# Kernel tuning notes

Hardware: AMD Instinct MI355X
Metric: run time of the kernel (lower is better)

The kernel has to match this reference:

```python
import jax, jax.numpy as jnp
import numpy as np

NUM_EXPERTS = 16
TOP_K = 2
FFT_LEN = 512
SEQ_LEN = 512
PRED_LEN = 720
MOE_TEMP = 1.0


def setup_inputs() -> dict:
    key = jax.random.key(0)
    ks = jax.random.split(key, 5)
    x = jax.random.normal(ks[0], (8192, SEQ_LEN), dtype=jnp.float32)
    # gating network: Linear(fft_len//2 -> num_experts)
    gw = jax.random.normal(ks[1], (NUM_EXPERTS, FFT_LEN // 2), dtype=jnp.float32) * (1.0 / np.sqrt(FFT_LEN // 2))
    gb = jnp.zeros((NUM_EXPERTS,), dtype=jnp.float32)
    # experts: RLinear = instance-norm (RevIN) + Linear(seq->pred), stacked
    ew = jax.random.normal(ks[2], (NUM_EXPERTS, SEQ_LEN, PRED_LEN), dtype=jnp.float32) * (1.0 / np.sqrt(SEQ_LEN))
    eb = jnp.zeros((NUM_EXPERTS, PRED_LEN), dtype=jnp.float32)
    return {"x": x, "gw": gw, "gb": gb, "ew": ew, "eb": eb}


def periodogram(x, n):
    # x: [B, L] -> normalized power spectrum [B, n//2]
    x0 = x - jnp.mean(x, axis=1, keepdims=True)
    dft = jnp.fft.fft(x0, n=n, axis=1) / jnp.sqrt(jnp.asarray(n, x.dtype))
    I = jnp.abs(dft[:, : n // 2]) ** 2
    s = jnp.sum(I, axis=1, keepdims=True)
    s = jnp.where(s == 0, 1.0, s)
    return I / s


def expert_apply(x, ew, eb):
    # RLinear: instance normalize, linear map, de-normalize
    mu = jnp.mean(x, axis=1, keepdims=True)
    sd = jnp.std(x, axis=1, keepdims=True) + 1e-5
    xn = (x - mu) / sd  # [B, L]
    # all experts densely: [B,L] x [E,L,P] -> [E,B,P]
    y = jnp.einsum('bl,elp->ebp', xn, ew) + eb[:, None, :]
    return y * sd[None] + mu[None]  # [E, B, P]


def reference(x, gw, gb, ew, eb):
    I = periodogram(x, FFT_LEN)  # [B, n//2]
    gate = (I @ gw.T + gb) / MOE_TEMP  # eval mode: divide by temp, no noise
    topk_vals, topk_idx = jax.lax.top_k(gate, TOP_K)  # [B, k]
    gates = jax.nn.softmax(topk_vals, axis=1)  # [B, k]
    expert_out = expert_apply(x, ew, eb)  # [E, B, P]
    # gather selected experts: [B, k, P]
    sel = jnp.take_along_axis(
        jnp.transpose(expert_out, (1, 0, 2)), topk_idx[:, :, None], axis=1
    )
    return jnp.sum(gates[:, :, None] * sel, axis=1)  # [B, P]
```

## Files before the change

### kernel.cpp

```cpp
#include <hip/hip_runtime.h>
#include <hip/hip_bf16.h>
#include <math.h>

#define NEXP  16
#define SEQ   512
#define PRED  720
#define NROWS 8192
#define NFREQ 256

typedef __bf16 bf16x8 __attribute__((ext_vector_type(8)));
typedef float  f32x16 __attribute__((ext_vector_type(16)));

__device__ __forceinline__ void gload_lds16(const void* g, void* l) {
    __builtin_amdgcn_global_load_lds(
        (const __attribute__((address_space(1))) unsigned int*)g,
        (__attribute__((address_space(3))) unsigned int*)l, 16, 0, 0);
}

__device__ __forceinline__ int xcd_swizzle(int bid, int nwg) {
    const int q = nwg >> 3, r = nwg & 7;
    const int xcd = bid & 7, off = bid >> 3;
    return (xcd < r ? xcd * (q + 1) : r * (q + 1) + (xcd - r) * q) + off;
}

__global__ __launch_bounds__(256) void k_transpose_ew(const float* __restrict__ ew,
                                                      __hip_bfloat16* __restrict__ ewt)
{
    __shared__ float tile[32][33];
    const int e  = blockIdx.z;
    const int p0 = blockIdx.x * 32;
    const int l0 = blockIdx.y * 32;
    const int tx = threadIdx.x & 31;
    const int ty = threadIdx.x >> 5;
    const float* src = ew + (size_t)e * SEQ * PRED;
#pragma unroll
    for (int i = 0; i < 4; ++i) {
        int l = l0 + ty + i * 8;
        int p = p0 + tx;
        tile[ty + i * 8][tx] = (p < PRED) ? src[(size_t)l * PRED + p] : 0.f;
    }
    __syncthreads();
    __hip_bfloat16* dst = ewt + (size_t)e * PRED * SEQ;
#pragma unroll
    for (int i = 0; i < 4; ++i) {
        int p = p0 + ty + i * 8;
        int l = l0 + tx;
        if (p < PRED) dst[(size_t)p * SEQ + l] = __float2bfloat16(tile[tx][ty + i * 8]);
    }
}

__global__ __launch_bounds__(256) void k_build_dft(__hip_bfloat16* __restrict__ bthi,
                                                   __hip_bfloat16* __restrict__ btlo,
                                                   int* __restrict__ nredo)
{
    if (blockIdx.x == 0 && threadIdx.x == 0) *nredo = 0;

    const int tid  = blockIdx.x * 256 + threadIdx.x;
    const int f    = tid >> 9;
    const int lidx = tid & 511;
    const int m    = (f * lidx) & 511;

    constexpr double Cj[9] = {0.9999247018391445033, 0.9996988186962042201,
                              0.9987954562051723927, 0.9951847266721968862,
                              0.9807852804032304491, 0.9238795325112867561,
                              0.7071067811865475244, 0.0, -1.0};
    constexpr double Sj[9] = {0.0122715382857199261, 0.0245412285229122880,
                              0.0490676743274180143, 0.0980171403295606020,
                              0.1950903220161282678, 0.3826834323650897717,
                              0.7071067811865475244, 1.0, 0.0};
    double cr = 1.0, ci = 0.0;
#pragma unroll
    for (int j = 0; j < 9; ++j) {
        const bool on = (m >> j) & 1;
        const double mr = on ? Cj[j] : 1.0;
        const double mi = on ? Sj[j] : 0.0;
        const double nr = cr * mr - ci * mi;
        ci = cr * mi + ci * mr;
        cr = nr;
    }

    const size_t c0 = (size_t)(2 * f) * 512 + lidx;
    const size_t c1 = (size_t)(2 * f + 1) * 512 + lidx;
    {
        __hip_bfloat16 h = __float2bfloat16((float)cr);
        float hif = __bfloat162float(h);
        bthi[c0] = h;
        btlo[c0] = __float2bfloat16((float)(cr - (double)hif));
    }
    {
        __hip_bfloat16 h = __float2bfloat16((float)ci);
        float hif = __bfloat162float(h);
        bthi[c1] = h;
        btlo[c1] = __float2bfloat16((float)(ci - (double)hif));
    }
}

__global__ __launch_bounds__(256) void k_stats(const float* __restrict__ x,
                                               __hip_bfloat16* __restrict__ xn,
                                               __hip_bfloat16* __restrict__ xnlo,
                                               float* __restrict__ meta)
{
    const int t  = threadIdx.x;
    const int wv = t >> 6, l = t & 63;
    const int b  = blockIdx.x * 4 + wv;
    const float* xr = x + (size_t)b * SEQ;

    const float4 v0 = *(const float4*)(xr + l * 8);
    const float4 v1 = *(const float4*)(xr + l * 8 + 4);
    const double d0 = v0.x, d1 = v0.y, d2 = v0.z, d3 = v0.w;
    const double d4 = v1.x, d5 = v1.y, d6 = v1.z, d7 = v1.w;

    double s1 = ((d0 + d1) + (d2 + d3)) + ((d4 + d5) + (d6 + d7));
    double s2 = ((d0 * d0 + d1 * d1) + (d2 * d2 + d3 * d3)) +
                ((d4 * d4 + d5 * d5) + (d6 * d6 + d7 * d7));
#pragma unroll
    for (int off = 1; off < 64; off <<= 1) {
        s1 += __shfl_xor(s1, off);
        s2 += __shfl_xor(s2, off);
    }
    const double mu = s1 * (1.0 / 512.0);
    double var = s2 * (1.0 / 512.0) - mu * mu;
    if (var < 0.0) var = 0.0;
    const double sd = sqrt(var) + 1e-5, inv = 1.0 / sd;

    unsigned int hw[4], lw[4];
#define CONV(j, dj)                                                         \
    {                                                                       \
        double xnd = (dj - mu) * inv;                                       \
        __hip_bfloat16 h = __float2bfloat16((float)xnd);                    \
        float hif = __bfloat162float(h);                                    \
        __hip_bfloat16 lo = __float2bfloat16((float)(xnd - (double)hif));   \
        unsigned int hb = *(unsigned short*)&h;                             \
        unsigned int lb = *(unsigned short*)&lo;                            \
        if ((j & 1) == 0) { hw[j >> 1] = hb; lw[j >> 1] = lb; }             \
        else { hw[j >> 1] |= hb << 16; lw[j >> 1] |= lb << 16; }            \
    }
    CONV(0, d0) CONV(1, d1) CONV(2, d2) CONV(3, d3)
    CONV(4, d4) CONV(5, d5) CONV(6, d6) CONV(7, d7)
#undef CONV
    *(uint4*)(xn   + (size_t)b * SEQ + l * 8) = uint4{hw[0], hw[1], hw[2], hw[3]};
    *(uint4*)(xnlo + (size_t)b * SEQ + l * 8) = uint4{lw[0], lw[1], lw[2], lw[3]};

    if (l == 0) {
        meta[b * 4 + 0] = (float)mu;
        meta[b * 4 + 3] = (float)sd;
    }
}

__global__ __launch_bounds__(256, 3) void k_dft_gemm(
    const __hip_bfloat16* __restrict__ xn, const __hip_bfloat16* __restrict__ xnlo,
    const __hip_bfloat16* __restrict__ bthi, const __hip_bfloat16* __restrict__ btlo,
    float* __restrict__ Iout)
{
    const int wgid = xcd_swizzle(blockIdx.x, 512);
    const int rt = wgid >> 2;
    const int ct = wgid & 3;

    __shared__ __align__(16) __hip_bfloat16 As[2][64][64];
    __shared__ __align__(16) __hip_bfloat16 Bs[2][128][64];

    const int t  = threadIdx.x;
    const int wv = t >> 6, l = t & 63;
    const int trow = t >> 3, tchk = t & 7;

    size_t aoff[2], boff[4];
#pragma unroll
    for (int i = 0; i < 2; ++i) {
        const int r   = i * 32 + trow;
        const int swz = (r & 7) ^ ((r & 8) >> 1);
        aoff[i] = (size_t)(rt * 64 + r) * SEQ + (size_t)(tchk ^ swz) * 8;
    }
#pragma unroll
    for (int i = 0; i < 4; ++i) {
        const int r   = i * 32 + trow;
        const int swz = (r & 7) ^ ((r & 8) >> 1);
        boff[i] = (size_t)(ct * 128 + r) * SEQ + (size_t)(tchk ^ swz) * 8;
    }

#define DSTAGE(buf, kk) do {                                                   \
    const int pass_ = (kk) >> 3;                                               \
    const int koff_ = ((kk) & 7) * 64;                                         \
    const __hip_bfloat16* ap_ = (pass_ == 1) ? xnlo : xn;                      \
    const __hip_bfloat16* bp_ = (pass_ == 2) ? btlo : bthi;                    \
    _Pragma("unroll")                                                          \
    for (int i_ = 0; i_ < 2; ++i_)                                             \
        gload_lds16(ap_ + aoff[i_] + koff_, &As[buf][i_ * 32 + wv * 8][0]);    \
    _Pragma("unroll")                                                          \
    for (int i_ = 0; i_ < 4; ++i_)                                             \
        gload_lds16(bp_ + boff[i_] + koff_, &Bs[buf][i_ * 32 + wv * 8][0]);    \
} while (0)

    f32x16 acc[2];
#pragma unroll
    for (int ni = 0; ni < 2; ++ni)
#pragma unroll
        for (int q = 0; q < 16; ++q) acc[ni][q] = 0.f;

    const int wr = wv >> 1, wc = wv & 1;
    const int fl = l & 31, fh = l >> 5;
    const int rswz = (fl & 7) ^ ((fl & 8) >> 1);

    DSTAGE(0, 0);
    DSTAGE(1, 1);
    for (int kt = 0; kt < 24; ++kt) {
        const int cur = kt & 1;
        if (kt < 23) asm volatile("s_waitcnt vmcnt(6)" ::: "memory");
        else         asm volatile("s_waitcnt vmcnt(0)" ::: "memory");
        __builtin_amdgcn_sched_barrier(0);
        __builtin_amdgcn_s_barrier();
        __builtin_amdgcn_sched_barrier(0);
#pragma unroll
        for (int ks = 0; ks < 4; ++ks) {
            const int g  = ks * 2 + fh;
            const int cc = (g ^ rswz) * 8;
            const bf16x8 a  = *(const bf16x8*)&As[cur][wr * 32 + fl][cc];
            const bf16x8 b0 = *(const bf16x8*)&Bs[cur][wc * 64 + fl][cc];
            const bf16x8 b1 = *(const bf16x8*)&Bs[cur][wc * 64 + 32 + fl][cc];
            acc[0] = __builtin_amdgcn_mfma_f32_32x32x16_bf16(a, b0, acc[0], 0, 0, 0);
            acc[1] = __builtin_amdgcn_mfma_f32_32x32x16_bf16(a, b1, acc[1], 0, 0, 0);
        }
        __builtin_amdgcn_sched_barrier(0);
        __builtin_amdgcn_s_barrier();
        __builtin_amdgcn_sched_barrier(0);
        if (kt + 2 < 24) DSTAGE(cur, kt + 2);
    }
#undef DSTAGE

    const int crow_base = 4 * fh;
#pragma unroll
    for (int ni = 0; ni < 2; ++ni) {
        const int col = ct * 128 + wc * 64 + ni * 32 + fl;
#pragma unroll
        for (int q = 0; q < 16; ++q) {
            const float v = acc[ni][q];
            const float w = __shfl_xor(v, 1);
            if ((fl & 1) == 0) {
                const int rl = wr * 32 + (q & 3) + 8 * (q >> 2) + crow_base;
                Iout[(size_t)(rt * 64 + rl) * NFREQ + (col >> 1)] = v * v + w * w;
            }
        }
    }
}

__global__ __launch_bounds__(256) void k_gatefin(const float* __restrict__ Iout,
                                                 const float* __restrict__ gw,
                                                 const float* __restrict__ gb,
                                                 float* __restrict__ meta,
                                                 int* __restrict__ eidx,
                                                 int* __restrict__ redo,
                                                 int* __restrict__ nredo)
{
    __shared__ float gws[NEXP * 257];
    __shared__ float Pw[4][256];
    __shared__ float Gs[4][16];

    const int t  = threadIdx.x;
    const int wv = t >> 6, l = t & 63;
    const int b  = blockIdx.x * 4 + wv;

    for (int i = t; i < NEXP * NFREQ; i += 256)
        gws[(i >> 8) * 257 + (i & 255)] = gw[i];
    __syncthreads();

    const float* Ir = Iout + (size_t)b * NFREQ;
    const float i0 = Ir[l], i1 = Ir[64 + l], i2 = Ir[128 + l], i3 = Ir[192 + l];
    Pw[wv][l] = i0; Pw[wv][64 + l] = i1; Pw[wv][128 + l] = i2; Pw[wv][192 + l] = i3;
    float ps = (i0 + i1) + (i2 + i3);
#pragma unroll
    for (int off = 1; off < 64; off <<= 1) ps += __shfl_xor(ps, off);

    const int e = l >> 2, kb = l & 3;
    float acc = 0.f;
#pragma unroll 8
    for (int j = 0; j < 64; ++j) {
        const int k = kb + 4 * j;
        acc += Pw[wv][k] * gws[e * 257 + k];
    }
    acc += __shfl_xor(acc, 1);
    acc += __shfl_xor(acc, 2);
    if (kb == 0) Gs[wv][e] = acc;

    if (l == 0) {
        const float sdiv  = (ps == 0.f) ? 1.f : ps;
        const float inv_s = 1.f / sdiv;
        float b1 = -1e30f, b2 = -1e30f, b3 = -1e30f;
        int i1b = 0, i2b = 0;
#pragma unroll
        for (int i = 0; i < NEXP; ++i) {
            float v = Gs[wv][i] * inv_s + gb[i];
            if (v > b1)      { b3 = b2; b2 = b1; i2b = i1b; b1 = v; i1b = i; }
            else if (v > b2) { b3 = b2; b2 = v; i2b = i; }
            else if (v > b3) { b3 = v; }
        }
        if (b2 - b3 < 1e-4f * fmaxf(1.f, fabsf(b1))) {
            const int r = atomicAdd(nredo, 1);
            redo[r] = b;
        } else {
            const float sd = meta[b * 4 + 3];
            const float ee = __expf(b2 - b1);
            const float w0 = 1.f / (1.f + ee);
            const float w1 = ee / (1.f + ee);
            meta[b * 4 + 1] = w0 * sd;
            meta[b * 4 + 2] = w1 * sd;
            eidx[b * 2 + 0] = i1b;
            eidx[b * 2 + 1] = i2b;
        }
    }
}

__global__ __launch_bounds__(256, 4) void k_gate64(const float* __restrict__ x,
                                                   const float* __restrict__ gw,
                                                   const float* __restrict__ gb,
                                                   float* __restrict__ meta,
                                                   int* __restrict__ eidx,
                                                   const int* __restrict__ redo,
                                                   const int* __restrict__ nredo)
{
    __shared__ double Pw[4][256];
    __shared__ double Gs[4][16];

    const int t  = threadIdx.x;
    const int wv = t >> 6, l = t & 63;
    const int n  = *nredo;

    for (int it = blockIdx.x * 4 + wv; it < n; it += gridDim.x * 4) {
        const int b = redo[it];
        const float* xr = x + (size_t)b * SEQ;

        double s1 = 0.0, s2 = 0.0;
#define DLOADV(n_) double vr##n_ = (double)xr[64 * n_ + l]; s1 += vr##n_; s2 += vr##n_ * vr##n_;
        DLOADV(0) DLOADV(1) DLOADV(2) DLOADV(3) DLOADV(4) DLOADV(5) DLOADV(6) DLOADV(7)
#undef DLOADV
        double vi0, vi1, vi2, vi3, vi4, vi5, vi6, vi7;

#pragma unroll
        for (int off = 1; off < 64; off <<= 1) {
            s1 += __shfl_xor(s1, off);
            s2 += __shfl_xor(s2, off);
        }
        const double mu = s1 * (1.0 / 512.0);
        double var = s2 * (1.0 / 512.0) - mu * mu;
        if (var < 0.0) var = 0.0;
        const double sd = sqrt(var) + 1e-5;

#define DSUB(n_) vr##n_ -= mu;
        DSUB(0) DSUB(1) DSUB(2) DSUB(3) DSUB(4) DSUB(5) DSUB(6) DSUB(7)
#undef DSUB

        {
            const double C = 0.70710678118654752440084436210485;
            double a0 = vr0 + vr4, a1 = vr1 + vr5, a2 = vr2 + vr6, a3 = vr3 + vr7;
            double d0 = vr0 - vr4, d1 = vr1 - vr5, d2 = vr2 - vr6, d3 = vr3 - vr7;
            double c0 = a0 + a2, c2 = a0 - a2, c1 = a1 + a3;
            double c3i = a3 - a1;
            double e1r = C * (d1 - d3), e1i = -C * (d1 + d3);
            vr0 = c0 + c1;   vi0 = 0.0;
            vr1 = c0 - c1;   vi1 = 0.0;
            vr2 = c2;        vi2 = c3i;
            vr3 = c2;        vi3 = -c3i;
            vr4 = d0 + e1r;  vi4 = -d2 + e1i;
            vr5 = d0 - e1r;  vi5 = -d2 - e1i;
            vr6 = d0 - e1r;  vi6 =  d2 + e1i;
            vr7 = d0 + e1r;  vi7 =  d2 - e1i;
        }

        double w1r = 1.0, w1i = 0.0;
        {
            constexpr double Cr[6] = {0.9999247018391445033, 0.9996988186962042201,
                                      0.9987954562051723927, 0.9951847266721968862,
                                      0.9807852804032304491, 0.9238795325112867561};
            constexpr double Ci[6] = {-0.0122715382857199261, -0.0245412285229122880,
                                      -0.0490676743274180143, -0.0980171403295606020,
                                      -0.1950903220161282678, -0.3826834323650897717};
#pragma unroll
            for (int j = 0; j < 6; ++j) {
                const bool on = (l >> j) & 1;
                const double mr = on ? Cr[j] : 1.0;
                const double mi = on ? Ci[j] : 0.0;
                const double nr = w1r * mr - w1i * mi;
                w1i = w1r * mi + w1i * mr;
                w1r = nr;
            }
        }

        {
            double wkr = w1r, wki = w1i;
#define DTWID(n_) { double tr_ = vr##n_ * wkr - vi##n_ * wki; \
                    vi##n_ = vr##n_ * wki + vi##n_ * wkr; vr##n_ = tr_; }
#define DWSTEP() { double nr_ = wkr * w1r - wki * w1i; \
                   wki = wkr * w1i + wki * w1r; wkr = nr_; }
            DTWID(4) DWSTEP() DTWID(2) DWSTEP() DTWID(6) DWSTEP() DTWID(1)
            DWSTEP() DTWID(5) DWSTEP() DTWID(3) DWSTEP() DTWID(7)
#undef DTWID
#undef DWSTEP
        }

        double twr, twi;
        {
            double w2r = w1r * w1r - w1i * w1i, w2i = 2.0 * w1r * w1i;
            double w4r = w2r * w2r - w2i * w2i, w4i = 2.0 * w2r * w2i;
            twr = w4r * w4r - w4i * w4i; twi = 2.0 * w4r * w4i;
        }
#define DBF(R, I, h, hi, ter, tei) { \
        double br_ = __shfl_xor(R, h); double bi_ = __shfl_xor(I, h); \
        double dr_ = hi ? (R - br_) : (R + br_); \
        double di_ = hi ? (I - bi_) : (I + bi_); \
        R = dr_ * ter - di_ * tei; I = dr_ * tei + di_ * ter; }
#define DSTAGE(hc) { \
        const bool hi_ = (l & hc) != 0; \
        const double ter_ = hi_ ? twr : 1.0; \
        const double tei_ = hi_ ? twi : 0.0; \
        DBF(vr0, vi0, hc, hi_, ter_, tei_) DBF(vr1, vi1, hc, hi_, ter_, tei_) \
        DBF(vr2, vi2, hc, hi_, ter_, tei_) DBF(vr3, vi3, hc, hi_, ter_, tei_) \
        DBF(vr4, vi4, hc, hi_, ter_, tei_) DBF(vr5, vi5, hc, hi_, ter_, tei_) \
        DBF(vr6, vi6, hc, hi_, ter_, tei_) DBF(vr7, vi7, hc, hi_, ter_, tei_) \
        double ntr_ = twr * twr - twi * twi; twi = 2.0 * twr * twi; twr = ntr_; }
        DSTAGE(32) DSTAGE(16) DSTAGE(8) DSTAGE(4) DSTAGE(2) DSTAGE(1)
#undef DSTAGE
#undef DBF

        const int k2 = (int)(__brev((unsigned)l) >> 26);
        double ps = 0.0;
        if ((l & 1) == 0) {
            const int kb = 8 * k2;
            double P;
            P = vr0 * vr0 + vi0 * vi0; ps += P; Pw[wv][0 + kb] = P;
            P = vr1 * vr1 + vi1 * vi1; ps += P; Pw[wv][4 + kb] = P;
            P = vr2 * vr2 + vi2 * vi2; ps += P; Pw[wv][2 + kb] = P;
            P = vr3 * vr3 + vi3 * vi3; ps += P; Pw[wv][6 + kb] = P;
            P = vr4 * vr4 + vi4 * vi4; ps += P; Pw[wv][1 + kb] = P;
            P = vr5 * vr5 + vi5 * vi5; ps += P; Pw[wv][5 + kb] = P;
            P = vr6 * vr6 + vi6 * vi6; ps += P; Pw[wv][3 + kb] = P;
            P = vr7 * vr7 + vi7 * vi7; ps += P; Pw[wv][7 + kb] = P;
        }
#pragma unroll
        for (int off = 1; off < 64; off <<= 1) ps += __shfl_xor(ps, off);

        {
            const int e = l >> 2, kb = l & 3;
            double acc = 0.0;
#pragma unroll 8
            for (int j = 0; j < 64; ++j) {
                int k = kb + 4 * j;
                acc += Pw[wv][k] * (double)gw[e * NFREQ + k];
            }
            acc += __shfl_xor(acc, 1);
            acc += __shfl_xor(acc, 2);
            if (kb == 0) Gs[wv][e] = acc;
        }

        if (l == 0) {
            const double sdiv  = (ps == 0.0) ? 1.0 : ps;
            const double inv_s = 1.0 / sdiv;
            double best = -1e300, best2 = -1e300;
            int i0b = 0, i1b = 0;
#pragma unroll
            for (int i = 0; i < NEXP; ++i) {
                double v = Gs[wv][i] * inv_s + (double)gb[i];
                if (v > best)       { best2 = best; i1b = i0b; best = v; i0b = i; }
                else if (v > best2) { best2 = v; i1b = i; }
            }
            const double eexp = (double)__expf((float)(best2 - best));
            const double w0 = 1.0 / (1.0 + eexp);
            const double w1 = eexp / (1.0 + eexp);
            meta[b * 4 + 0] = (float)mu;
            meta[b * 4 + 1] = (float)(w0 * sd);
            meta[b * 4 + 2] = (float)(w1 * sd);
            meta[b * 4 + 3] = (float)sd;
            eidx[b * 2 + 0] = i0b;
            eidx[b * 2 + 1] = i1b;
        }
    }
}

__global__ __launch_bounds__(256) void k_count(const int* __restrict__ eidx,
                                               int* __restrict__ blockHist)
{
    __shared__ int h[32];
    const int t   = threadIdx.x;
    const int blk = blockIdx.x;
    if (t < 32) h[t] = 0;
    __syncthreads();
    const int b  = blk * 256 + t;
    const int e0 = eidx[2 * b];
    const int e1 = eidx[2 * b + 1];
    atomicAdd(&h[e0], 1);
    atomicAdd(&h[16 + e1], 1);
    __syncthreads();
    if (t < 32) blockHist[(t >> 4) * 512 + blk * 16 + (t & 15)] = h[t];
}

__global__ void k_scan(const int* __restrict__ blockHist, int* __restrict__ counts,
                       int* __restrict__ offs, int* __restrict__ toff,
                       int* __restrict__ base)
{
    __shared__ int cnt[32];
    __shared__ int off_s[32];
    const int j = threadIdx.x;
    if (j < 32) {
        const int s = j >> 4, e = j & 15;
        int acc = 0;
        for (int blk = 0; blk < 32; ++blk) acc += blockHist[s * 512 + blk * 16 + e];
        cnt[j] = acc;
        counts[j] = acc;
    }
    __syncthreads();
    if (j < 2) {
        int acc = 0, tac = 0;
        for (int i = 0; i < NEXP; ++i) {
            const int c = cnt[j * 16 + i];
            off_s[j * 16 + i] = acc;
            offs[j * 16 + i]  = acc;
            acc += c;
            toff[j * 17 + i] = tac;
            tac += (c + 63) >> 6;
        }
        toff[j * 17 + 16] = tac;
    }
    __syncthreads();
    if (j < 32) {
        const int s = j >> 4, e = j & 15;
        int run = off_s[j];
        for (int blk = 0; blk < 32; ++blk) {
            base[s * 512 + blk * 16 + e] = run;
            run += blockHist[s * 512 + blk * 16 + e];
        }
    }
}

__global__ __launch_bounds__(256) void k_scatter(const int* __restrict__ eidx,
                                                 const int* __restrict__ base,
                                                 int* __restrict__ lists)
{
    __shared__ int whist[2][4][16];
    const int t   = threadIdx.x;
    const int wv  = t >> 6, l = t & 63;
    const int blk = blockIdx.x;
    const int b   = blk * 256 + t;
    const int e0  = eidx[2 * b];
    const int e1  = eidx[2 * b + 1];
    const unsigned long long before = (1ULL << l) - 1ULL;

    unsigned long long m0 = 0, m1 = 0;
#pragma unroll
    for (int bb = 0; bb < 16; ++bb) {
        unsigned long long m = __ballot(e0 == bb);
        if (e0 == bb) m0 = m;
        if (l == 0) whist[0][wv][bb] = __popcll(m);
    }
#pragma unroll
    for (int bb = 0; bb < 16; ++bb) {
        unsigned long long m = __ballot(e1 == bb);
        if (e1 == bb) m1 = m;
        if (l == 0) whist[1][wv][bb] = __popcll(m);
    }
    __syncthreads();

    int p0 = __popcll(m0 & before);
    int p1 = __popcll(m1 & before);
    for (int w = 0; w < 4; ++w) {
        if (w < wv) {
            p0 += whist[0][w][e0];
            p1 += whist[1][w][e1];
        }
    }
    lists[base[blk * 16 + e0] + p0]                 = b;
    lists[NROWS + base[512 + blk * 16 + e1] + p1]   = b;
}

template <int SLOT>
__global__ __launch_bounds__(256, 3) void k_expert_gemm(
    const __hip_bfloat16* __restrict__ xn, const __hip_bfloat16* __restrict__ ewt,
    const float* __restrict__ eb, const float* __restrict__ meta,
    const int* __restrict__ lists, const int* __restrict__ offs,
    const int* __restrict__ counts, const int* __restrict__ toff,
    float* __restrict__ out)
{
    const int wgid = xcd_swizzle(blockIdx.x, 864);
    const int tid  = wgid / 6;
    const int ct   = wgid % 6;
    if (tid >= toff[SLOT * 17 + 16]) return;
    int e = 0;
#pragma unroll
    for (int i = 0; i < 15; ++i) e += (toff[SLOT * 17 + e + 1] <= tid) ? 1 : 0;
    const int rt  = tid - toff[SLOT * 17 + e];
    const int n_e = counts[SLOT * NEXP + e];

    __shared__ __align__(16) __hip_bfloat16 As[2][64][64];
    __shared__ __align__(16) __hip_bfloat16 Bs[2][128][64];
    __shared__ int   rowB[64];
    __shared__ float rowMu[64];
    __shared__ float rowC[64];

    const int t  = threadIdx.x;
    const int wv = t >> 6, l = t & 63;
    const int* list = lists + SLOT * NROWS + offs[SLOT * NEXP + e];
    if (t < 64) {
        int r  = rt * 64 + t;
        int bb = (r < n_e) ? list[r] : -1;
        rowB[t]  = bb;
        rowMu[t] = (bb >= 0) ? meta[bb * 4] : 0.f;
        rowC[t]  = (bb >= 0) ? meta[bb * 4 + 1 + SLOT] : 0.f;
    }
    __syncthreads();

    const int trow = t >> 3, tchk = t & 7;
    const __hip_bfloat16* asrc[2];
    const __hip_bfloat16* bsrc[4];
#pragma unroll
    for (int i = 0; i < 2; ++i) {
        const int r   = i * 32 + trow;
        const int swz = (r & 7) ^ ((r & 8) >> 1);
        const int ab  = rowB[r];
        asrc[i] = xn + ((ab >= 0) ? (size_t)ab * SEQ : 0) + (size_t)(tchk ^ swz) * 8;
    }
#pragma unroll
    for (int i = 0; i < 4; ++i) {
        const int r   = i * 32 + trow;
        const int swz = (r & 7) ^ ((r & 8) >> 1);
        const int gc  = ct * 128 + r;
        const int gcc = (gc < PRED) ? gc : (PRED - 1);
        bsrc[i] = ewt + ((size_t)e * PRED + gcc) * SEQ + (size_t)(tchk ^ swz) * 8;
    }

#define STAGE(buf, koff) do {                                              \
    _Pragma("unroll")                                                      \
    for (int i_ = 0; i_ < 2; ++i_)                                         \
        gload_lds16(asrc[i_] + (koff), &As[buf][i_ * 32 + wv * 8][0]);     \
    _Pragma("unroll")                                                      \
    for (int i_ = 0; i_ < 4; ++i_)                                         \
        gload_lds16(bsrc[i_] + (koff), &Bs[buf][i_ * 32 + wv * 8][0]);     \
} while (0)

    f32x16 acc[2];
#pragma unroll
    for (int ni = 0; ni < 2; ++ni)
#pragma unroll
        for (int q = 0; q < 16; ++q) acc[ni][q] = 0.f;

    const int wr = wv >> 1, wc = wv & 1;
    const int fl = l & 31, fh = l >> 5;
    const int rswz = (fl & 7) ^ ((fl & 8) >> 1);

    STAGE(0, 0);
    STAGE(1, 64);
    for (int kt = 0; kt < 8; ++kt) {
        const int cur = kt & 1;
        if (kt < 7) asm volatile("s_waitcnt vmcnt(6)" ::: "memory");
        else        asm volatile("s_waitcnt vmcnt(0)" ::: "memory");
        __builtin_amdgcn_sched_barrier(0);
        __builtin_amdgcn_s_barrier();
        __builtin_amdgcn_sched_barrier(0);
#pragma unroll
        for (int ks = 0; ks < 4; ++ks) {
            const int g  = ks * 2 + fh;
            const int cc = (g ^ rswz) * 8;
            const bf16x8 a  = *(const bf16x8*)&As[cur][wr * 32 + fl][cc];
            const bf16x8 b0 = *(const bf16x8*)&Bs[cur][wc * 64 + fl][cc];
            const bf16x8 b1 = *(const bf16x8*)&Bs[cur][wc * 64 + 32 + fl][cc];
            acc[0] = __builtin_amdgcn_mfma_f32_32x32x16_bf16(a, b0, acc[0], 0, 0, 0);
            acc[1] = __builtin_amdgcn_mfma_f32_32x32x16_bf16(a, b1, acc[1], 0, 0, 0);
        }
        __builtin_amdgcn_sched_barrier(0);
        __builtin_amdgcn_s_barrier();
        __builtin_amdgcn_sched_barrier(0);
        if (kt + 2 < 8) STAGE(cur, (kt + 2) * 64);
    }
#undef STAGE

    const int crow_base = 4 * fh;
#pragma unroll
    for (int ni = 0; ni < 2; ++ni) {
        const int col = ct * 128 + wc * 64 + ni * 32 + fl;
        const bool cok = (col < PRED);
        const float ebv = cok ? eb[e * PRED + col] : 0.f;
#pragma unroll
        for (int q = 0; q < 16; ++q) {
            const int rl = wr * 32 + (q & 3) + 8 * (q >> 2) + crow_base;
            const int bb = rowB[rl];
            if (!cok || bb < 0) continue;
            const float v = acc[ni][q] + ebv;
            float* op = out + (size_t)bb * PRED + col;
            if (SLOT == 0) *op = rowMu[rl] + rowC[rl] * v;
            else           *op += rowC[rl] * v;
        }
    }
}

extern "C" void kernel_launch(void* const* d_in, const int* in_sizes, int n_in,
                              void* d_out, int out_size, void* d_ws, size_t ws_size,
                              hipStream_t stream)
{
    const float* x  = (const float*)d_in[0];
    const float* gw = (const float*)d_in[1];
    const float* gb = (const float*)d_in[2];
    const float* ew = (const float*)d_in[3];
    const float* eb = (const float*)d_in[4];
    float* out = (float*)d_out;
    char*  ws  = (char*)d_ws;

    constexpr size_t XN_OFF   = 0;
    constexpr size_t XN_SZ    = (size_t)NROWS * SEQ * 2;
    constexpr size_t XNLO_OFF = XN_OFF + XN_SZ;
    constexpr size_t EWT_OFF  = XNLO_OFF + XN_SZ;
    constexpr size_t EWT_SZ   = (size_t)NEXP * PRED * SEQ * 2;
    constexpr size_t BTHI_OFF = EWT_OFF + EWT_SZ;
    constexpr size_t BT_SZ    = (size_t)512 * 512 * 2;
    constexpr size_t BTLO_OFF = BTHI_OFF + BT_SZ;
    constexpr size_t IOUT_OFF = BTLO_OFF + BT_SZ;
    constexpr size_t IOUT_SZ  = (size_t)NROWS * NFREQ * 4;
    constexpr size_t META_OFF = IOUT_OFF + IOUT_SZ;
    constexpr size_t META_SZ  = (size_t)NROWS * 4 * 4;
    constexpr size_t EIDX_OFF = META_OFF + META_SZ;
    constexpr size_t EIDX_SZ  = (size_t)NROWS * 2 * 4;
    constexpr size_t LIST_OFF = EIDX_OFF + EIDX_SZ;
    constexpr size_t LIST_SZ  = (size_t)2 * NROWS * 4;
    constexpr size_t CNT_OFF  = LIST_OFF + LIST_SZ;
    constexpr size_t OFFS_OFF = CNT_OFF + 144;
    constexpr size_t TOFF_OFF = OFFS_OFF + 128;
    constexpr size_t BH_OFF   = TOFF_OFF + 160;
    constexpr size_t BASE_OFF = BH_OFF + 4096;
    constexpr size_t REDO_OFF = BASE_OFF + 4096;

    __hip_bfloat16* xn   = (__hip_bfloat16*)(ws + XN_OFF);
    __hip_bfloat16* xnlo = (__hip_bfloat16*)(ws + XNLO_OFF);
    __hip_bfloat16* ewt  = (__hip_bfloat16*)(ws + EWT_OFF);
    __hip_bfloat16* bthi = (__hip_bfloat16*)(ws + BTHI_OFF);
    __hip_bfloat16* btlo = (__hip_bfloat16*)(ws + BTLO_OFF);
    float* Iout  = (float*)(ws + IOUT_OFF);
    float* meta  = (float*)(ws + META_OFF);
    int* eidx    = (int*)(ws + EIDX_OFF);
    int* lists   = (int*)(ws + LIST_OFF);
    int* counts  = (int*)(ws + CNT_OFF);
    int* nredo   = (int*)(ws + CNT_OFF + 128);
    int* offs    = (int*)(ws + OFFS_OFF);
    int* toff    = (int*)(ws + TOFF_OFF);
    int* bhist   = (int*)(ws + BH_OFF);
    int* base    = (int*)(ws + BASE_OFF);
    int* redo    = (int*)(ws + REDO_OFF);

    k_build_dft<<<dim3(512), dim3(256), 0, stream>>>(bthi, btlo, nredo);
    k_transpose_ew<<<dim3(23, 16, NEXP), dim3(256), 0, stream>>>(ew, ewt);
    k_stats<<<dim3(NROWS / 4), dim3(256), 0, stream>>>(x, xn, xnlo, meta);
    k_dft_gemm<<<dim3(512), dim3(256), 0, stream>>>(xn, xnlo, bthi, btlo, Iout);
    k_gatefin<<<dim3(NROWS / 4), dim3(256), 0, stream>>>(Iout, gw, gb, meta, eidx,
                                                         redo, nredo);
    k_gate64<<<dim3(64), dim3(256), 0, stream>>>(x, gw, gb, meta, eidx, redo, nredo);
    k_count<<<dim3(32), dim3(256), 0, stream>>>(eidx, bhist);
    k_scan<<<dim3(1), dim3(64), 0, stream>>>(bhist, counts, offs, toff, base);
    k_scatter<<<dim3(32), dim3(256), 0, stream>>>(eidx, base, lists);
    k_expert_gemm<0><<<dim3(864), dim3(256), 0, stream>>>(
        xn, ewt, eb, meta, lists, offs, counts, toff, out);
    k_expert_gemm<1><<<dim3(864), dim3(256), 0, stream>>>(
        xn, ewt, eb, meta, lists, offs, counts, toff, out);
}
```

Baseline: 154.0 us.

## Shrink GEMM tiles to 64x64 and use triple-buffered LDS with one barrier

Both the DFT GEMM and the expert GEMM go from 64x128 output tiles to 64x64, which doubles the grid size, and move from double to triple LDS buffering. With three buffers the second barrier after each compute step is dropped, so each k-step has one barrier and the prefetch can be two stages ahead. The cost is lower data reuse per block (each A tile is loaded twice as often) and one accumulator per wave instead of two, which means fewer MFMAs per LDS load.

```diff
diff --git a/kernel.cpp b/kernel.cpp
--- a/kernel.cpp
+++ b/kernel.cpp
@@ -152,29 +152,26 @@
     const __hip_bfloat16* __restrict__ bthi, const __hip_bfloat16* __restrict__ btlo,
     float* __restrict__ Iout)
 {
-    const int wgid = xcd_swizzle(blockIdx.x, 512);
-    const int rt = wgid >> 2;
-    const int ct = wgid & 3;
-
-    __shared__ __align__(16) __hip_bfloat16 As[2][64][64];
-    __shared__ __align__(16) __hip_bfloat16 Bs[2][128][64];
+    const int wgid = xcd_swizzle(blockIdx.x, 1024);
+    const int rt = wgid >> 3;
+    const int ct = wgid & 7;
+
+    __shared__ __align__(16) __hip_bfloat16 As[3][64][64];
+    __shared__ __align__(16) __hip_bfloat16 Bs[3][64][64];
 
     const int t  = threadIdx.x;
     const int wv = t >> 6, l = t & 63;
-    const int trow = t >> 3, tchk = t & 7;
-
-    size_t aoff[2], boff[4];
+
+    size_t aoff[2], boff[2];
+    int ldsrow[2], ldschk[2];
 #pragma unroll
     for (int i = 0; i < 2; ++i) {
-        const int r   = i * 32 + trow;
-        const int swz = (r & 7) ^ ((r & 8) >> 1);
-        aoff[i] = (size_t)(rt * 64 + r) * SEQ + (size_t)(tchk ^ swz) * 8;
-    }
-#pragma unroll
-    for (int i = 0; i < 4; ++i) {
-        const int r   = i * 32 + trow;
-        const int swz = (r & 7) ^ ((r & 8) >> 1);
-        boff[i] = (size_t)(ct * 128 + r) * SEQ + (size_t)(tchk ^ swz) * 8;
+        const int idx = i * 256 + t;
+        const int row = idx >> 3, chk = idx & 7;
+        const int swz = (row & 7) ^ ((row & 8) >> 1);
+        ldsrow[i] = row; ldschk[i] = chk;
+        aoff[i] = (size_t)(rt * 64 + row) * SEQ + (size_t)(chk ^ swz) * 8;
+        boff[i] = (size_t)(ct * 64 + row) * SEQ + (size_t)(chk ^ swz) * 8;
     }
 
 #define DSTAGE(buf, kk) do {                                                   \
@@ -184,17 +181,15 @@
     const __hip_bfloat16* bp_ = (pass_ == 2) ? btlo : bthi;                    \
     _Pragma("unroll")                                                          \
     for (int i_ = 0; i_ < 2; ++i_)                                             \
-        gload_lds16(ap_ + aoff[i_] + koff_, &As[buf][i_ * 32 + wv * 8][0]);    \
+        gload_lds16(ap_ + aoff[i_] + koff_, &As[buf][ldsrow[i_]][ldschk[i_] * 8]); \
     _Pragma("unroll")                                                          \
-    for (int i_ = 0; i_ < 4; ++i_)                                             \
-        gload_lds16(bp_ + boff[i_] + koff_, &Bs[buf][i_ * 32 + wv * 8][0]);    \
+    for (int i_ = 0; i_ < 2; ++i_)                                             \
+        gload_lds16(bp_ + boff[i_] + koff_, &Bs[buf][ldsrow[i_]][ldschk[i_] * 8]); \
 } while (0)
 
-    f32x16 acc[2];
-#pragma unroll
-    for (int ni = 0; ni < 2; ++ni)
-#pragma unroll
-        for (int q = 0; q < 16; ++q) acc[ni][q] = 0.f;
+    f32x16 acc;
+#pragma unroll
+    for (int q = 0; q < 16; ++q) acc[q] = 0.f;
 
     const int wr = wv >> 1, wc = wv & 1;
     const int fl = l & 31, fh = l >> 5;
@@ -202,42 +197,34 @@
 
     DSTAGE(0, 0);
     DSTAGE(1, 1);
+#pragma unroll
     for (int kt = 0; kt < 24; ++kt) {
-        const int cur = kt & 1;
-        if (kt < 23) asm volatile("s_waitcnt vmcnt(6)" ::: "memory");
+        const int cur = kt % 3;
+        if (kt < 23) asm volatile("s_waitcnt vmcnt(4)" ::: "memory");
         else         asm volatile("s_waitcnt vmcnt(0)" ::: "memory");
         __builtin_amdgcn_sched_barrier(0);
         __builtin_amdgcn_s_barrier();
         __builtin_amdgcn_sched_barrier(0);
 #pragma unroll
         for (int ks = 0; ks < 4; ++ks) {
-            const int g  = ks * 2 + fh;
-            const int cc = (g ^ rswz) * 8;
-            const bf16x8 a  = *(const bf16x8*)&As[cur][wr * 32 + fl][cc];
-            const bf16x8 b0 = *(const bf16x8*)&Bs[cur][wc * 64 + fl][cc];
-            const bf16x8 b1 = *(const bf16x8*)&Bs[cur][wc * 64 + 32 + fl][cc];
-            acc[0] = __builtin_amdgcn_mfma_f32_32x32x16_bf16(a, b0, acc[0], 0, 0, 0);
-            acc[1] = __builtin_amdgcn_mfma_f32_32x32x16_bf16(a, b1, acc[1], 0, 0, 0);
-        }
-        __builtin_amdgcn_sched_barrier(0);
-        __builtin_amdgcn_s_barrier();
-        __builtin_amdgcn_sched_barrier(0);
-        if (kt + 2 < 24) DSTAGE(cur, kt + 2);
+            const int cc = ((ks * 2 + fh) ^ rswz) * 8;
+            const bf16x8 a = *(const bf16x8*)&As[cur][wr * 32 + fl][cc];
+            const bf16x8 b = *(const bf16x8*)&Bs[cur][wc * 32 + fl][cc];
+            acc = __builtin_amdgcn_mfma_f32_32x32x16_bf16(a, b, acc, 0, 0, 0);
+        }
+        if (kt + 2 < 24) DSTAGE((kt + 2) % 3, kt + 2);
     }
 #undef DSTAGE
 
     const int crow_base = 4 * fh;
-#pragma unroll
-    for (int ni = 0; ni < 2; ++ni) {
-        const int col = ct * 128 + wc * 64 + ni * 32 + fl;
-#pragma unroll
-        for (int q = 0; q < 16; ++q) {
-            const float v = acc[ni][q];
-            const float w = __shfl_xor(v, 1);
-            if ((fl & 1) == 0) {
-                const int rl = wr * 32 + (q & 3) + 8 * (q >> 2) + crow_base;
-                Iout[(size_t)(rt * 64 + rl) * NFREQ + (col >> 1)] = v * v + w * w;
-            }
+    const int col = ct * 64 + wc * 32 + fl;
+#pragma unroll
+    for (int q = 0; q < 16; ++q) {
+        const float v = acc[q];
+        const float w = __shfl_xor(v, 1);
+        if ((fl & 1) == 0) {
+            const int rl = wr * 32 + (q & 3) + 8 * (q >> 2) + crow_base;
+            Iout[(size_t)(rt * 64 + rl) * NFREQ + (col >> 1)] = v * v + w * w;
         }
     }
 }
@@ -406,7 +393,7 @@
         double dr_ = hi ? (R - br_) : (R + br_); \
         double di_ = hi ? (I - bi_) : (I + bi_); \
         R = dr_ * ter - di_ * tei; I = dr_ * tei + di_ * ter; }
-#define DSTAGE(hc) { \
+#define DSTG(hc) { \
         const bool hi_ = (l & hc) != 0; \
         const double ter_ = hi_ ? twr : 1.0; \
         const double tei_ = hi_ ? twi : 0.0; \
@@ -415,8 +402,8 @@
         DBF(vr4, vi4, hc, hi_, ter_, tei_) DBF(vr5, vi5, hc, hi_, ter_, tei_) \
         DBF(vr6, vi6, hc, hi_, ter_, tei_) DBF(vr7, vi7, hc, hi_, ter_, tei_) \
         double ntr_ = twr * twr - twi * twi; twi = 2.0 * twr * twi; twr = ntr_; }
-        DSTAGE(32) DSTAGE(16) DSTAGE(8) DSTAGE(4) DSTAGE(2) DSTAGE(1)
-#undef DSTAGE
+        DSTG(32) DSTG(16) DSTG(8) DSTG(4) DSTG(2) DSTG(1)
+#undef DSTG
 #undef DBF
 
         const int k2 = (int)(__brev((unsigned)l) >> 26);
@@ -576,9 +563,9 @@
     const int* __restrict__ counts, const int* __restrict__ toff,
     float* __restrict__ out)
 {
-    const int wgid = xcd_swizzle(blockIdx.x, 864);
-    const int tid  = wgid / 6;
-    const int ct   = wgid % 6;
+    const int wgid = xcd_swizzle(blockIdx.x, 1728);
+    const int tid  = wgid / 12;
+    const int ct   = wgid % 12;
     if (tid >= toff[SLOT * 17 + 16]) return;
     int e = 0;
 #pragma unroll
@@ -586,8 +573,8 @@
     const int rt  = tid - toff[SLOT * 17 + e];
     const int n_e = counts[SLOT * NEXP + e];
 
-    __shared__ __align__(16) __hip_bfloat16 As[2][64][64];
-    __shared__ __align__(16) __hip_bfloat16 Bs[2][128][64];
+    __shared__ __align__(16) __hip_bfloat16 As[3][64][64];
+    __shared__ __align__(16) __hip_bfloat16 Bs[3][64][64];
     __shared__ int   rowB[64];
     __shared__ float rowMu[64];
     __shared__ float rowC[64];
@@ -604,39 +591,34 @@
     }
     __syncthreads();
 
-    const int trow = t >> 3, tchk = t & 7;
     const __hip_bfloat16* asrc[2];
-    const __hip_bfloat16* bsrc[4];
+    const __hip_bfloat16* bsrc[2];
+    int ldsrow[2], ldschk[2];
 #pragma unroll
     for (int i = 0; i < 2; ++i) {
-        const int r   = i * 32 + trow;
-        const int swz = (r & 7) ^ ((r & 8) >> 1);
-        const int ab  = rowB[r];
-        asrc[i] = xn + ((ab >= 0) ? (size_t)ab * SEQ : 0) + (size_t)(tchk ^ swz) * 8;
-    }
-#pragma unroll
-    for (int i = 0; i < 4; ++i) {
-        const int r   = i * 32 + trow;
-        const int swz = (r & 7) ^ ((r & 8) >> 1);
-        const int gc  = ct * 128 + r;
+        const int idx = i * 256 + t;
+        const int row = idx >> 3, chk = idx & 7;
+        const int swz = (row & 7) ^ ((row & 8) >> 1);
+        ldsrow[i] = row; ldschk[i] = chk;
+        const int ab  = rowB[row];
+        asrc[i] = xn + ((ab >= 0) ? (size_t)ab * SEQ : 0) + (size_t)(chk ^ swz) * 8;
+        const int gc  = ct * 64 + row;
         const int gcc = (gc < PRED) ? gc : (PRED - 1);
-        bsrc[i] = ewt + ((size_t)e * PRED + gcc) * SEQ + (size_t)(tchk ^ swz) * 8;
-    }
-
-#define STAGE(buf, koff) do {                                              \
-    _Pragma("unroll")                                                      \
-    for (int i_ = 0; i_ < 2; ++i_)                                         \
-        gload_lds16(asrc[i_] + (koff), &As[buf][i_ * 32 + wv * 8][0]);     \
-    _Pragma("unroll")                                                      \
-    for (int i_ = 0; i_ < 4; ++i_)                                         \
-        gload_lds16(bsrc[i_] + (koff), &Bs[buf][i_ * 32 + wv * 8][0]);     \
+        bsrc[i] = ewt + ((size_t)e * PRED + gcc) * SEQ + (size_t)(chk ^ swz) * 8;
+    }
+
+#define STAGE(buf, koff) do {                                                      \
+    _Pragma("unroll")                                                              \
+    for (int i_ = 0; i_ < 2; ++i_)                                                 \
+        gload_lds16(asrc[i_] + (koff), &As[buf][ldsrow[i_]][ldschk[i_] * 8]);      \
+    _Pragma("unroll")                                                              \
+    for (int i_ = 0; i_ < 2; ++i_)                                                 \
+        gload_lds16(bsrc[i_] + (koff), &Bs[buf][ldsrow[i_]][ldschk[i_] * 8]);      \
 } while (0)
 
-    f32x16 acc[2];
-#pragma unroll
-    for (int ni = 0; ni < 2; ++ni)
-#pragma unroll
-        for (int q = 0; q < 16; ++q) acc[ni][q] = 0.f;
+    f32x16 acc;
+#pragma unroll
+    for (int q = 0; q < 16; ++q) acc[q] = 0.f;
 
     const int wr = wv >> 1, wc = wv & 1;
     const int fl = l & 31, fh = l >> 5;
@@ -644,46 +626,38 @@
 
     STAGE(0, 0);
     STAGE(1, 64);
+#pragma unroll
     for (int kt = 0; kt < 8; ++kt) {
-        const int cur = kt & 1;
-        if (kt < 7) asm volatile("s_waitcnt vmcnt(6)" ::: "memory");
+        const int cur = kt % 3;
+        if (kt < 7) asm volatile("s_waitcnt vmcnt(4)" ::: "memory");
         else        asm volatile("s_waitcnt vmcnt(0)" ::: "memory");
         __builtin_amdgcn_sched_barrier(0);
         __builtin_amdgcn_s_barrier();
         __builtin_amdgcn_sched_barrier(0);
 #pragma unroll
         for (int ks = 0; ks < 4; ++ks) {
-            const int g  = ks * 2 + fh;
-            const int cc = (g ^ rswz) * 8;
-            const bf16x8 a  = *(const bf16x8*)&As[cur][wr * 32 + fl][cc];
-            const bf16x8 b0 = *(const bf16x8*)&Bs[cur][wc * 64 + fl][cc];
-            const bf16x8 b1 = *(const bf16x8*)&Bs[cur][wc * 64 + 32 + fl][cc];
-            acc[0] = __builtin_amdgcn_mfma_f32_32x32x16_bf16(a, b0, acc[0], 0, 0, 0);
-            acc[1] = __builtin_amdgcn_mfma_f32_32x32x16_bf16(a, b1, acc[1], 0, 0, 0);
-        }
-        __builtin_amdgcn_sched_barrier(0);
-        __builtin_amdgcn_s_barrier();
-        __builtin_amdgcn_sched_barrier(0);
-        if (kt + 2 < 8) STAGE(cur, (kt + 2) * 64);
+            const int cc = ((ks * 2 + fh) ^ rswz) * 8;
+            const bf16x8 a = *(const bf16x8*)&As[cur][wr * 32 + fl][cc];
+            const bf16x8 b = *(const bf16x8*)&Bs[cur][wc * 32 + fl][cc];
+            acc = __builtin_amdgcn_mfma_f32_32x32x16_bf16(a, b, acc, 0, 0, 0);
+        }
+        if (kt + 2 < 8) STAGE((kt + 2) % 3, (kt + 2) * 64);
     }
 #undef STAGE
 
     const int crow_base = 4 * fh;
-#pragma unroll
-    for (int ni = 0; ni < 2; ++ni) {
-        const int col = ct * 128 + wc * 64 + ni * 32 + fl;
-        const bool cok = (col < PRED);
-        const float ebv = cok ? eb[e * PRED + col] : 0.f;
-#pragma unroll
-        for (int q = 0; q < 16; ++q) {
-            const int rl = wr * 32 + (q & 3) + 8 * (q >> 2) + crow_base;
-            const int bb = rowB[rl];
-            if (!cok || bb < 0) continue;
-            const float v = acc[ni][q] + ebv;
-            float* op = out + (size_t)bb * PRED + col;
-            if (SLOT == 0) *op = rowMu[rl] + rowC[rl] * v;
-            else           *op += rowC[rl] * v;
-        }
+    const int col = ct * 64 + wc * 32 + fl;
+    const bool cok = (col < PRED);
+    const float ebv = cok ? eb[e * PRED + col] : 0.f;
+#pragma unroll
+    for (int q = 0; q < 16; ++q) {
+        const int rl = wr * 32 + (q & 3) + 8 * (q >> 2) + crow_base;
+        const int bb = rowB[rl];
+        if (!cok || bb < 0) continue;
+        const float v = acc[q] + ebv;
+        float* op = out + (size_t)bb * PRED + col;
+        if (SLOT == 0) *op = rowMu[rl] + rowC[rl] * v;
+        else           *op += rowC[rl] * v;
     }
 }
 
@@ -742,15 +716,15 @@
     k_build_dft<<<dim3(512), dim3(256), 0, stream>>>(bthi, btlo, nredo);
     k_transpose_ew<<<dim3(23, 16, NEXP), dim3(256), 0, stream>>>(ew, ewt);
     k_stats<<<dim3(NROWS / 4), dim3(256), 0, stream>>>(x, xn, xnlo, meta);
-    k_dft_gemm<<<dim3(512), dim3(256), 0, stream>>>(xn, xnlo, bthi, btlo, Iout);
+    k_dft_gemm<<<dim3(1024), dim3(256), 0, stream>>>(xn, xnlo, bthi, btlo, Iout);
     k_gatefin<<<dim3(NROWS / 4), dim3(256), 0, stream>>>(Iout, gw, gb, meta, eidx,
                                                          redo, nredo);
     k_gate64<<<dim3(64), dim3(256), 0, stream>>>(x, gw, gb, meta, eidx, redo, nredo);
     k_count<<<dim3(32), dim3(256), 0, stream>>>(eidx, bhist);
     k_scan<<<dim3(1), dim3(64), 0, stream>>>(bhist, counts, offs, toff, base);
     k_scatter<<<dim3(32), dim3(256), 0, stream>>>(eidx, base, lists);
-    k_expert_gemm<0><<<dim3(864), dim3(256), 0, stream>>>(
+    k_expert_gemm<0><<<dim3(1728), dim3(256), 0, stream>>>(
         xn, ewt, eb, meta, lists, offs, counts, toff, out);
-    k_expert_gemm<1><<<dim3(864), dim3(256), 0, stream>>>(
+    k_expert_gemm<1><<<dim3(1728), dim3(256), 0, stream>>>(
         xn, ewt, eb, meta, lists, offs, counts, toff, out);
 }
```

Measured after the change: 150.5 us. 1.02x faster.
